# Performance work log

Measured on AMD Instinct MI355X. Metric: run time of the kernel, lower is better.

The kernel has to match this reference:

```python
import jax, jax.numpy as jnp
import numpy as np

B, M, HS, K = 2, 2048, 1024, 16
D = HS // K


def setup_inputs() -> dict:
    key = jax.random.key(0)
    k1, k2, k3, k4 = jax.random.split(key, 4)
    s = 1.0 / np.sqrt(HS)
    return {
        "h": jax.random.normal(k1, (B, M, HS), jnp.float32),
        "W_span": jax.random.normal(k2, (2 * K, HS), jnp.float32) * s,
        "W_val": jax.random.normal(k3, (HS, HS), jnp.float32) * s,
        "W_out": jax.random.normal(k4, (HS, HS), jnp.float32) * s,
    }


def _head_reshape(x, d):
    # (B, M, K*d) -> (B*K, M, d), matching torch view/transpose in head_reshape
    b, m, _ = x.shape
    return x.reshape(b, m, K, d).transpose(0, 2, 1, 3).reshape(b * K, m, d)


def reference(h, W_span, W_val, W_out):
    b, m, hs = h.shape
    span = _head_reshape(h @ W_span.T, 2)        # (B*K, M, 2)
    value = _head_reshape(h @ W_val.T, D)        # (B*K, M, D)
    # AutoSelectAttention: learned per-position Gaussian span over absolute positions
    pos = jnp.arange(m, dtype=h.dtype)           # (M,)
    mean = jax.nn.sigmoid(span[..., 0]) * m      # (B*K, M) span center in [0, M]
    soft = jax.nn.softplus(span[..., 1])         # (B*K, M) sharpness >= 0
    diff = pos[None, None, :] - mean[..., None]  # (B*K, M, M)
    scores = -soft[..., None] * (diff * diff)
    attn = jax.nn.softmax(scores, axis=-1)       # (B*K, M, M)
    out = jnp.matmul(attn, value)                # (B*K, M, D)
    out = out.reshape(b, K, m, D).transpose(0, 2, 1, 3).reshape(b, m, hs)
    return out @ W_out.T
```

## Files before the change

### kernel.cpp

```cpp
#include <hip/hip_runtime.h>
#include <hip/hip_bf16.h>

#define MM   2048
#define HSZ  1024
#define KH   16
#define DH   64

typedef __attribute__((ext_vector_type(8))) short bf16x8;
typedef __attribute__((ext_vector_type(4))) float f32x4;
typedef __attribute__((ext_vector_type(8))) unsigned short u16x8;

#define GLOAD_LDS16(gp, lp) \
    __builtin_amdgcn_global_load_lds( \
        (const __attribute__((address_space(1))) unsigned int*)(gp), \
        (__attribute__((address_space(3))) unsigned int*)(lp), 16, 0, 0)

__device__ __forceinline__ unsigned short f2bf(float x) {
    union { float f; unsigned u; } v; v.f = x;
    unsigned r = v.u + 0x7FFFu + ((v.u >> 16) & 1u);
    return (unsigned short)(r >> 16);
}

__global__ __launch_bounds__(256) void span_cvt(
    const float* __restrict__ h, const float* __restrict__ Wspan,
    const float* __restrict__ Wval, const float* __restrict__ Wout,
    float* __restrict__ mean_, float* __restrict__ soft_,
    unsigned short* __restrict__ h_bf,
    unsigned short* __restrict__ Wval_bf, unsigned short* __restrict__ Wout_bf)
{
    __shared__ float hrow[4][HSZ];
    int t = threadIdx.x;

    if (blockIdx.x >= 1024) {
        int bid = blockIdx.x - 1024;
        const float* in = (bid < 1024) ? Wval : Wout;
        unsigned short* out = (bid < 1024) ? Wval_bf : Wout_bf;
        int i = ((bid & 1023) * 256 + t) * 4;
        float4 v = *(const float4*)(in + i);
        ushort4 o;
        o.x = f2bf(v.x); o.y = f2bf(v.y); o.z = f2bf(v.z); o.w = f2bf(v.w);
        *(ushort4*)(out + i) = o;
        return;
    }

    int row0 = blockIdx.x * 4;
    #pragma unroll
    for (int i = 0; i < 4; ++i) {
        int li = t + 256 * i;
        int r = li >> 8, c4 = (li & 255) * 4;
        float4 hv = *(const float4*)&h[(long)(row0 + r) * HSZ + c4];
        *(float4*)&hrow[r][c4] = hv;
        ushort4 hb;
        hb.x = f2bf(hv.x); hb.y = f2bf(hv.y); hb.z = f2bf(hv.z); hb.w = f2bf(hv.w);
        *(ushort4*)&h_bf[(long)(row0 + r) * HSZ + c4] = hb;
    }
    __syncthreads();
    int o = t >> 3, part = t & 7;
    const float* w = Wspan + o * HSZ;
    float4 acc[4] = {};
    #pragma unroll 4
    for (int i = 0; i < 32; ++i) {
        int c = part * 4 + i * 32;
        float4 wv = *(const float4*)&w[c];
        #pragma unroll
        for (int r = 0; r < 4; ++r) {
            float4 a = *(const float4*)&hrow[r][c];
            acc[r].x += a.x * wv.x; acc[r].y += a.y * wv.y;
            acc[r].z += a.z * wv.z; acc[r].w += a.w * wv.w;
        }
    }
    #pragma unroll
    for (int r = 0; r < 4; ++r) {
        float s = acc[r].x + acc[r].y + acc[r].z + acc[r].w;
        s += __shfl_xor(s, 1, 64);
        s += __shfl_xor(s, 2, 64);
        s += __shfl_xor(s, 4, 64);
        if (part == 0) {
            int m = row0 + r;
            int b = m >> 11, mm = m & 2047;
            int bk = b * KH + (o >> 1);
            if ((o & 1) == 0) {
                mean_[bk * MM + mm] = (1.f / (1.f + __expf(-s))) * (float)MM;
            } else {
                float sp = (s > 15.f) ? s : log1pf(__expf(s));
                soft_[bk * MM + mm] = sp;
            }
        }
    }
}

#define SROW(li) ((li) >> 3)
#define SCOL(li) ((((li) & 7) ^ (SROW(li) & 7)) * 8)

template<int STORE_BF16>
__device__ __forceinline__ void gemm_core64(
    unsigned short* __restrict__ AsB, unsigned short* __restrict__ BsB,
    const unsigned short* __restrict__ A, const unsigned short* __restrict__ Bm,
    void* __restrict__ Cv, int N, int Kd,
    int bx, int by, int bz, long aZ, long bZ, long cZ)
{
    const unsigned short* Ab = A  + bz * aZ;
    const unsigned short* Bb = Bm + bz * bZ;
    long czoff = bz * cZ;
    int row0 = by * 64;
    int col0 = bx * 64;
    int t = threadIdx.x;
    int wid = t >> 6, l = t & 63;
    int wr = wid >> 1, wc = wid & 1;
    int lr = l & 15, lhi = l >> 4;

    #define STAGE64(buf, k0s) do { \
        unsigned short* As_ = AsB + (buf) * 4096; \
        unsigned short* Bs_ = BsB + (buf) * 4096; \
        int a0 = t, a1 = t + 256; \
        GLOAD_LDS16(Ab + (long)(row0 + SROW(a0)) * Kd + (k0s) + SCOL(a0), As_ + a0 * 8); \
        GLOAD_LDS16(Ab + (long)(row0 + SROW(a1)) * Kd + (k0s) + SCOL(a1), As_ + a1 * 8); \
        GLOAD_LDS16(Bb + (long)(col0 + SROW(a0)) * Kd + (k0s) + SCOL(a0), Bs_ + a0 * 8); \
        GLOAD_LDS16(Bb + (long)(col0 + SROW(a1)) * Kd + (k0s) + SCOL(a1), Bs_ + a1 * 8); \
    } while (0)

    f32x4 acc[2][2] = {};
    int nk = Kd >> 6;

    STAGE64(0, 0);

    for (int ks = 0; ks < nk; ++ks) {
        int cur = ks & 1;
        if (ks + 1 < nk) {
            STAGE64(cur ^ 1, (ks + 1) << 6);
            asm volatile("s_waitcnt vmcnt(4)" ::: "memory");
        } else {
            asm volatile("s_waitcnt vmcnt(0)" ::: "memory");
        }
        __builtin_amdgcn_s_barrier();

        bf16x8 af[2][2], bfr[2][2];
        #pragma unroll
        for (int kk = 0; kk < 2; ++kk) {
            int slotx = ((kk * 4 + lhi) ^ (lr & 7)) << 3;
            #pragma unroll
            for (int i = 0; i < 2; ++i)
                af[kk][i] = *(const bf16x8*)(AsB + cur * 4096 + (wr * 32 + i * 16 + lr) * 64 + slotx);
            #pragma unroll
            for (int j = 0; j < 2; ++j)
                bfr[kk][j] = *(const bf16x8*)(BsB + cur * 4096 + (wc * 32 + j * 16 + lr) * 64 + slotx);
        }
        asm volatile("s_waitcnt lgkmcnt(0)" ::: "memory");
        __builtin_amdgcn_sched_barrier(0);
        __builtin_amdgcn_s_barrier();

        #pragma unroll
        for (int kk = 0; kk < 2; ++kk)
            #pragma unroll
            for (int i = 0; i < 2; ++i)
                #pragma unroll
                for (int j = 0; j < 2; ++j)
                    acc[i][j] = __builtin_amdgcn_mfma_f32_16x16x32_bf16(af[kk][i], bfr[kk][j], acc[i][j], 0, 0, 0);
    }
    #undef STAGE64

    #pragma unroll
    for (int i = 0; i < 2; ++i) {
        int rbase = row0 + wr * 32 + i * 16 + lhi * 4;
        #pragma unroll
        for (int j = 0; j < 2; ++j) {
            int cidx = col0 + wc * 32 + j * 16 + lr;
            #pragma unroll
            for (int r_ = 0; r_ < 4; ++r_) {
                long idx = czoff + (long)(rbase + r_) * N + cidx;
                if (STORE_BF16) ((unsigned short*)Cv)[idx] = f2bf(acc[i][j][r_]);
                else            ((float*)Cv)[idx] = acc[i][j][r_];
            }
        }
    }
}

__device__ void sort_core(char* smem, const float* __restrict__ mean_,
                          int* __restrict__ perm, int bk)
{
    unsigned short (*hist)[257] = (unsigned short(*)[257])smem;
    int* binTot = (int*)(smem + 16448);
    int* binStart = binTot + 32;
    int t = threadIdx.x;
    int bins[8];
    #pragma unroll
    for (int i = 0; i < 8; ++i) {
        float mq = mean_[bk * MM + t * 8 + i];
        int b = (int)(mq * (1.f / 64.f));
        bins[i] = min(31, max(0, b));
    }
    for (int b = 0; b < 32; ++b) hist[b][t] = 0;
    __syncthreads();
    #pragma unroll
    for (int i = 0; i < 8; ++i) hist[bins[i]][t]++;
    __syncthreads();
    int w = t >> 6, l = t & 63;
    for (int b = w * 8; b < w * 8 + 8; ++b) {
        int carry = 0;
        for (int g = 0; g < 4; ++g) {
            int v = (int)hist[b][g * 64 + l];
            int x = v;
            #pragma unroll
            for (int off = 1; off < 64; off <<= 1) {
                int y = __shfl_up(x, off, 64);
                if (l >= off) x += y;
            }
            hist[b][g * 64 + l] = (unsigned short)(x - v + carry);
            carry += __shfl(x, 63, 64);
        }
        if (l == 0) binTot[b] = carry;
    }
    __syncthreads();
    if (t == 0) {
        int s = 0;
        for (int b = 0; b < 32; ++b) { binStart[b] = s; s += binTot[b]; }
    }
    __syncthreads();
    #pragma unroll
    for (int i = 0; i < 8; ++i) {
        int b = bins[i];
        int prior = 0;
        #pragma unroll
        for (int j = 0; j < 8; ++j) if (j < i && bins[j] == b) prior++;
        int pos = binStart[b] + (int)hist[b][t] + prior;
        perm[bk * MM + pos] = t * 8 + i;
    }
}

__global__ __launch_bounds__(256) void vgemm_sort(
    const unsigned short* __restrict__ Wval_bf, const unsigned short* __restrict__ h_bf,
    unsigned short* __restrict__ hvT,
    const float* __restrict__ mean_, int* __restrict__ perm)
{
    __shared__ __align__(16) char smem[32768];
    int f = blockIdx.x;
    if (f < 1024) {
        int swz = (f & 7) * 128 + (f >> 3);
        int by = swz & 15, r = swz >> 4;
        int bx = r & 31, bz = r >> 5;
        gemm_core64<1>((unsigned short*)smem, (unsigned short*)(smem + 16384),
                       Wval_bf, h_bf, hvT, MM, HSZ, bx, by, bz,
                       0L, (long)MM * HSZ, (long)HSZ * MM);
    } else {
        sort_core(smem, mean_, perm, f - 1024);
    }
}

__global__ __launch_bounds__(256) void ogemm(
    const unsigned short* __restrict__ att, const unsigned short* __restrict__ Wout_bf,
    float* __restrict__ out)
{
    __shared__ __align__(16) unsigned short As[2][4096];
    __shared__ __align__(16) unsigned short Bs[2][4096];
    int f = blockIdx.x;
    int swz = (f & 7) * 128 + (f >> 3);
    int bx = swz & 15, by = (swz >> 4) & 63;
    gemm_core64<0>(&As[0][0], &Bs[0][0], att, Wout_bf, out, HSZ, HSZ,
                   bx, by, 0, 0L, 0L, 0L);
}

__global__ __launch_bounds__(512) void attn_gauss(
    const float* __restrict__ mean_, const float* __restrict__ soft_,
    const int* __restrict__ perm,
    const unsigned short* __restrict__ hvT, unsigned short* __restrict__ att)
{
    __shared__ __align__(16) unsigned short Vs[2][64 * 64];
    __shared__ float red[2][8];
    int flat = blockIdx.x;
    int swz = (flat & 7) * 64 + (flat >> 3);
    int bk = swz >> 4;
    int qb = swz & 15;
    int t = threadIdx.x, wid = t >> 6, l = t & 63;
    int b = bk >> 4, head = bk & 15;
    int lr = l & 15, lhi = l >> 4;
    int slot = qb * 128 + wid * 16 + lr;
    int q = perm[bk * MM + slot];
    float mq  = mean_[bk * MM + q];
    float sq  = soft_[bk * MM + q];
    const unsigned short* Vbase = hvT + (long)bk * DH * MM;

    float w = __fsqrt_rn(50.f / sq);
    float lo = mq - w, hi = mq + w;
    #pragma unroll
    for (int off = 1; off < 64; off <<= 1) {
        lo = fminf(lo, __shfl_xor(lo, off, 64));
        hi = fmaxf(hi, __shfl_xor(hi, off, 64));
    }
    if (l == 0) { red[0][wid] = lo; red[1][wid] = hi; }
    __syncthreads();
    float blo = red[0][0], bhi = red[1][0];
    #pragma unroll
    for (int i = 1; i < 8; ++i) {
        blo = fminf(blo, red[0][i]);
        bhi = fmaxf(bhi, red[1][i]);
    }
    blo = fmaxf(blo, 0.f);
    bhi = fmaxf(fminf(bhi, 2047.f), 0.f);
    int kt0 = ((int)blo) >> 6;
    int kt1 = ((int)bhi) >> 6;
    if (kt1 < kt0) kt1 = kt0;

    int sr = t >> 3;
    int sc = (((t & 7) ^ (sr & 7)) * 8);

    f32x4 acc[4] = {};
    float lsum = 0.f;
    int jlane0 = lhi * 8;

    GLOAD_LDS16(Vbase + (long)sr * MM + (kt0 << 6) + sc, &Vs[0][t * 8]);
    __syncthreads();

    for (int kt = kt0; kt <= kt1; ++kt) {
        int cur = (kt - kt0) & 1;
        int k0 = kt << 6;
        if (kt < kt1)
            GLOAD_LDS16(Vbase + (long)sr * MM + (k0 + 64) + sc, &Vs[cur ^ 1][t * 8]);

        float dmin = fmaxf(fmaxf((float)k0 - mq, mq - (float)(k0 + 63)), 0.f);
        bool active = (sq * dmin * dmin) < 50.f;
        if (__ballot(active)) {
            #pragma unroll
            for (int kk = 0; kk < 64; kk += 32) {
                bf16x8 pfrag;
                float dbase = (float)(k0 + kk + jlane0) - mq;
                #pragma unroll
                for (int jj = 0; jj < 8; ++jj) {
                    float d_ = dbase + (float)jj;
                    float p = __expf(-sq * d_ * d_);
                    lsum += p;
                    pfrag[jj] = (short)f2bf(p);
                }
                int slotx = (((kk >> 3) + lhi) ^ (lr & 7)) << 3;
                #pragma unroll
                for (int df = 0; df < 4; ++df) {
                    bf16x8 vf = *(const bf16x8*)&Vs[cur][(df * 16 + lr) * 64 + slotx];
                    acc[df] = __builtin_amdgcn_mfma_f32_16x16x32_bf16(pfrag, vf, acc[df], 0, 0, 0);
                }
            }
        }
        __syncthreads();
    }

    lsum += __shfl_xor(lsum, 16, 64);
    lsum += __shfl_xor(lsum, 32, 64);

    int slot_base = qb * 128 + wid * 16;
    #pragma unroll
    for (int r_ = 0; r_ < 4; ++r_) {
        int qr = lhi * 4 + r_;
        float inv = 1.f / __shfl(lsum, qr, 64);
        int qo = perm[bk * MM + slot_base + qr];
        long orow = ((long)b * MM + qo) * HSZ + head * DH;
        #pragma unroll
        for (int df = 0; df < 4; ++df)
            att[orow + df * 16 + lr] = f2bf(acc[df][r_] * inv);
    }
}

extern "C" void kernel_launch(void* const* d_in, const int* in_sizes, int n_in,
                              void* d_out, int out_size, void* d_ws, size_t ws_size,
                              hipStream_t stream) {
    (void)in_sizes; (void)n_in; (void)out_size; (void)ws_size;
    const float* h     = (const float*)d_in[0];
    const float* Wspan = (const float*)d_in[1];
    const float* Wval  = (const float*)d_in[2];
    const float* Wout  = (const float*)d_in[3];
    float* out = (float*)d_out;

    char* ws = (char*)d_ws;
    unsigned short* h_bf    = (unsigned short*)(ws);
    unsigned short* Wval_bf = (unsigned short*)(ws +  8388608);
    unsigned short* Wout_bf = (unsigned short*)(ws + 10485760);
    unsigned short* hvT     = (unsigned short*)(ws + 12582912);
    unsigned short* att     = (unsigned short*)(ws + 20971520);
    float*          mean_   = (float*)(ws + 29360128);
    float*          soft_   = (float*)(ws + 29622272);
    int*            perm    = (int*)(ws + 29884416);

    span_cvt<<<3072, 256, 0, stream>>>(h, Wspan, Wval, Wout,
                                       mean_, soft_, h_bf, Wval_bf, Wout_bf);

    vgemm_sort<<<1056, 256, 0, stream>>>(Wval_bf, h_bf, hvT, mean_, perm);

    attn_gauss<<<512, 512, 0, stream>>>(mean_, soft_, perm, hvT, att);

    ogemm<<<1024, 256, 0, stream>>>(att, Wout_bf, out);
}
```

Baseline: 66.39 us.

## Compute span projection with split-bf16 MFMA and decouple conversion blocks

The span projection h@W_span^T moves from scalar FP32 dot products over an LDS-staged row to MFMA bf16 instructions. Each FP32 operand is split into high and low bf16 parts and three MFMAs are summed to keep near-FP32 accuracy. The four waves each cover a quarter of the K dimension and are reduced through shared memory. The bf16 conversion of h, Wval and Wout now runs in separate blocks that each handle four float4s per thread, giving 1792 blocks instead of 3072. In exchange, h is read twice (once for the span projection and once for conversion) and the split-bf16 product carries a small precision risk.

```diff
diff --git a/kernel.cpp b/kernel.cpp
--- a/kernel.cpp
+++ b/kernel.cpp
@@ -21,71 +21,87 @@
     return (unsigned short)(r >> 16);
 }
 
-__global__ __launch_bounds__(256) void span_cvt(
+__global__ __launch_bounds__(256) void pre_fused(
     const float* __restrict__ h, const float* __restrict__ Wspan,
     const float* __restrict__ Wval, const float* __restrict__ Wout,
     float* __restrict__ mean_, float* __restrict__ soft_,
     unsigned short* __restrict__ h_bf,
     unsigned short* __restrict__ Wval_bf, unsigned short* __restrict__ Wout_bf)
 {
-    __shared__ float hrow[4][HSZ];
+    __shared__ float red[4][16][33];
     int t = threadIdx.x;
 
-    if (blockIdx.x >= 1024) {
-        int bid = blockIdx.x - 1024;
-        const float* in = (bid < 1024) ? Wval : Wout;
-        unsigned short* out = (bid < 1024) ? Wval_bf : Wout_bf;
-        int i = ((bid & 1023) * 256 + t) * 4;
-        float4 v = *(const float4*)(in + i);
-        ushort4 o;
-        o.x = f2bf(v.x); o.y = f2bf(v.y); o.z = f2bf(v.z); o.w = f2bf(v.w);
-        *(ushort4*)(out + i) = o;
+    if (blockIdx.x >= 256) {
+        int bid = blockIdx.x - 256;
+        #pragma unroll
+        for (int i = 0; i < 4; ++i) {
+            int fi = bid * 1024 + i * 256 + t;
+            const float* in; unsigned short* out; int off;
+            if (fi < 1048576)      { in = h;    out = h_bf;    off = fi; }
+            else if (fi < 1310720) { in = Wval; out = Wval_bf; off = fi - 1048576; }
+            else                   { in = Wout; out = Wout_bf; off = fi - 1310720; }
+            float4 v = *(const float4*)(in + (long)off * 4);
+            ushort4 o4;
+            o4.x = f2bf(v.x); o4.y = f2bf(v.y); o4.z = f2bf(v.z); o4.w = f2bf(v.w);
+            *(ushort4*)(out + (long)off * 4) = o4;
+        }
         return;
     }
 
-    int row0 = blockIdx.x * 4;
-    #pragma unroll
-    for (int i = 0; i < 4; ++i) {
-        int li = t + 256 * i;
-        int r = li >> 8, c4 = (li & 255) * 4;
-        float4 hv = *(const float4*)&h[(long)(row0 + r) * HSZ + c4];
-        *(float4*)&hrow[r][c4] = hv;
-        ushort4 hb;
-        hb.x = f2bf(hv.x); hb.y = f2bf(hv.y); hb.z = f2bf(hv.z); hb.w = f2bf(hv.w);
-        *(ushort4*)&h_bf[(long)(row0 + r) * HSZ + c4] = hb;
-    }
-    __syncthreads();
-    int o = t >> 3, part = t & 7;
-    const float* w = Wspan + o * HSZ;
-    float4 acc[4] = {};
-    #pragma unroll 4
-    for (int i = 0; i < 32; ++i) {
-        int c = part * 4 + i * 32;
-        float4 wv = *(const float4*)&w[c];
-        #pragma unroll
-        for (int r = 0; r < 4; ++r) {
-            float4 a = *(const float4*)&hrow[r][c];
-            acc[r].x += a.x * wv.x; acc[r].y += a.y * wv.y;
-            acc[r].z += a.z * wv.z; acc[r].w += a.w * wv.w;
-        }
-    }
-    #pragma unroll
-    for (int r = 0; r < 4; ++r) {
-        float s = acc[r].x + acc[r].y + acc[r].z + acc[r].w;
-        s += __shfl_xor(s, 1, 64);
-        s += __shfl_xor(s, 2, 64);
-        s += __shfl_xor(s, 4, 64);
-        if (part == 0) {
-            int m = row0 + r;
-            int b = m >> 11, mm = m & 2047;
-            int bk = b * KH + (o >> 1);
-            if ((o & 1) == 0) {
-                mean_[bk * MM + mm] = (1.f / (1.f + __expf(-s))) * (float)MM;
-            } else {
-                float sp = (s > 15.f) ? s : log1pf(__expf(s));
-                soft_[bk * MM + mm] = sp;
-            }
-        }
+    int blk = blockIdx.x;
+    int wid = t >> 6, l = t & 63;
+    int lr = l & 15, lhi = l >> 4;
+    int m0 = blk * 16;
+    const float* hrow = h + (long)(m0 + lr) * HSZ + wid * 256;
+
+    f32x4 acc[2] = {};
+
+    #define SPLIT8(af_, hh_, hl_) { \
+        _Pragma("unroll") for (int j_ = 0; j_ < 8; ++j_) { \
+            unsigned short hu_ = f2bf(af_[j_]); \
+            union { unsigned u; float f; } cv_; cv_.u = (unsigned)hu_ << 16; \
+            hh_[j_] = (short)hu_; hl_[j_] = (short)f2bf(af_[j_] - cv_.f); } }
+
+    #pragma unroll
+    for (int ks = 0; ks < 8; ++ks) {
+        int k0 = ks * 32 + lhi * 8;
+        float4 a0 = *(const float4*)(hrow + k0);
+        float4 a1 = *(const float4*)(hrow + k0 + 4);
+        float af[8] = {a0.x, a0.y, a0.z, a0.w, a1.x, a1.y, a1.z, a1.w};
+        bf16x8 hh, hl;
+        SPLIT8(af, hh, hl);
+        #pragma unroll
+        for (int ct = 0; ct < 2; ++ct) {
+            const float* wrow = Wspan + (long)(ct * 16 + lr) * HSZ + wid * 256 + k0;
+            float4 w0 = *(const float4*)wrow;
+            float4 w1 = *(const float4*)(wrow + 4);
+            float wf[8] = {w0.x, w0.y, w0.z, w0.w, w1.x, w1.y, w1.z, w1.w};
+            bf16x8 wh, wl;
+            SPLIT8(wf, wh, wl);
+            acc[ct] = __builtin_amdgcn_mfma_f32_16x16x32_bf16(hh, wh, acc[ct], 0, 0, 0);
+            acc[ct] = __builtin_amdgcn_mfma_f32_16x16x32_bf16(hh, wl, acc[ct], 0, 0, 0);
+            acc[ct] = __builtin_amdgcn_mfma_f32_16x16x32_bf16(hl, wh, acc[ct], 0, 0, 0);
+        }
+    }
+    #undef SPLIT8
+
+    #pragma unroll
+    for (int ct = 0; ct < 2; ++ct)
+        #pragma unroll
+        for (int r_ = 0; r_ < 4; ++r_)
+            red[wid][lhi * 4 + r_][ct * 16 + lr] = acc[ct][r_];
+    __syncthreads();
+
+    int r = t >> 4, o2 = t & 15;
+    #pragma unroll
+    for (int half = 0; half < 2; ++half) {
+        int o = half * 16 + o2;
+        float s = red[0][r][o] + red[1][r][o] + red[2][r][o] + red[3][r][o];
+        int m = m0 + r;
+        int bb = m >> 11, mm = m & 2047;
+        int bk = bb * KH + (o >> 1);
+        if (!(o & 1)) mean_[bk * MM + mm] = (1.f / (1.f + __expf(-s))) * (float)MM;
+        else          soft_[bk * MM + mm] = (s > 15.f) ? s : log1pf(__expf(s));
     }
 }
 
@@ -377,8 +393,8 @@
     float*          soft_   = (float*)(ws + 29622272);
     int*            perm    = (int*)(ws + 29884416);
 
-    span_cvt<<<3072, 256, 0, stream>>>(h, Wspan, Wval, Wout,
-                                       mean_, soft_, h_bf, Wval_bf, Wout_bf);
+    pre_fused<<<1792, 256, 0, stream>>>(h, Wspan, Wval, Wout,
+                                        mean_, soft_, h_bf, Wval_bf, Wout_bf);
 
     vgemm_sort<<<1056, 256, 0, stream>>>(Wval_bf, h_bf, hvT, mean_, perm);
 
```

After: 65.96 us, median of 3. About the same (-0.6%).
